# Kernel tuning notes

Hardware: AMD Instinct MI355X
Metric: run time of the kernel (lower is better)

The kernel has to match this reference:

```python
import jax, jax.numpy as jnp
import numpy as np
import math

B, S, H = 2, 2048, 2048
NH, HD = 16, 64  # head_dim = H // (2*NH)
LAMBDA_INIT = 0.5


def setup_inputs() -> dict:
    key = jax.random.key(0)
    ks = jax.random.split(key, 6)
    std = 1.0 / math.sqrt(H)
    hidden_states = jax.random.normal(ks[0], (B, S, H), dtype=jnp.float32)
    # Linear weights stored as [in, out] (x @ W)
    Wq = jax.random.normal(ks[1], (H, 2 * NH * HD), dtype=jnp.float32) * std
    Wk = jax.random.normal(ks[2], (H, 2 * NH * HD), dtype=jnp.float32) * std
    Wv = jax.random.normal(ks[3], (H, NH * HD), dtype=jnp.float32) * std
    Wo = jax.random.normal(ks[4], (NH * HD, H), dtype=jnp.float32) * (1.0 / math.sqrt(NH * HD))
    lambda_param = jnp.log(jnp.asarray(1.0 / math.tanh(LAMBDA_INIT), dtype=jnp.float32))
    # causal additive mask, (B, 1, S, S)
    causal = jnp.tril(jnp.ones((S, S), dtype=bool))
    attention_mask = jnp.where(causal, 0.0, jnp.finfo(jnp.float32).min)[None, None]
    attention_mask = jnp.broadcast_to(attention_mask, (B, 1, S, S))
    return {"hidden_states": hidden_states, "attention_mask": attention_mask,
            "Wq": Wq, "Wk": Wk, "Wv": Wv, "Wo": Wo, "lambda_param": lambda_param}


def reference(hidden_states, attention_mask, Wq, Wk, Wv, Wo, lambda_param):
    bsz, q_len, _ = hidden_states.shape
    scaling = HD ** -0.5

    q_all = (hidden_states @ Wq).reshape(bsz, q_len, 2 * NH, HD).transpose(0, 2, 1, 3)
    k_all = (hidden_states @ Wk).reshape(bsz, q_len, 2 * NH, HD).transpose(0, 2, 1, 3)
    v = (hidden_states @ Wv).reshape(bsz, q_len, NH, HD).transpose(0, 2, 1, 3)
    q1, q2 = q_all[:, :NH], q_all[:, NH:]
    k1, k2 = k_all[:, :NH], k_all[:, NH:]

    lam = jnp.tanh(jax.nn.softplus(lambda_param))
    scores1 = jnp.einsum('bhqd,bhkd->bhqk', q1, k1) * scaling
    scores2 = jnp.einsum('bhqd,bhkd->bhqk', q2, k2) * scaling
    attn_scores = scores1 - lam * scores2 + attention_mask
    attn_weights = jax.nn.softmax(attn_scores.astype(jnp.float32), axis=-1).astype(q1.dtype)

    attn_out = jnp.einsum('bhqk,bhkd->bhqd', attn_weights, v)
    attn_out = attn_out.transpose(0, 2, 1, 3).reshape(bsz, q_len, NH * HD)
    return attn_out @ Wo
```

## Files before the change

kernel.cpp:

```cpp
#include <hip/hip_runtime.h>
#include <hip/hip_bf16.h>

#define B_ 2
#define S_ 2048
#define H_ 2048
#define NH_ 16
#define HD_ 64
#define DQ_ 2048
#define DV_ 1024

using bf16x8 = __attribute__((ext_vector_type(8))) __bf16;
using f32x4  = __attribute__((ext_vector_type(4))) float;

typedef __attribute__((address_space(1))) unsigned int u32g;
typedef __attribute__((address_space(3))) unsigned int u32l;

__device__ __forceinline__ void gload_lds16(const __bf16* g, __bf16* l) {
  __builtin_amdgcn_global_load_lds((u32g*)g, (u32l*)l, 16, 0, 0);
}

__device__ __forceinline__ int swz(int row, int colb, int strideB) {
  return row * strideB + (colb ^ (((row ^ (row >> 3)) & 7) << 4));
}
__device__ __forceinline__ int fxor(int row) { return (row ^ (row >> 3)) & 7; }


__global__ __launch_bounds__(256) void cast_hidden(const float* __restrict__ in,
                                                   __bf16* __restrict__ out, int n) {
  int i = (blockIdx.x * 256 + threadIdx.x) * 8;
  if (i >= n) return;
  float4 a = *reinterpret_cast<const float4*>(in + i);
  float4 b = *reinterpret_cast<const float4*>(in + i + 4);
  bf16x8 o;
  o[0] = (__bf16)a.x; o[1] = (__bf16)a.y; o[2] = (__bf16)a.z; o[3] = (__bf16)a.w;
  o[4] = (__bf16)b.x; o[5] = (__bf16)b.y; o[6] = (__bf16)b.z; o[7] = (__bf16)b.w;
  *reinterpret_cast<bf16x8*>(out + i) = o;
}

__global__ __launch_bounds__(256) void transpose_cast(const float* __restrict__ in,
                                                      __bf16* __restrict__ out, int R, int C) {
  __shared__ float tile[32][33];
  int tx = threadIdx.x & 31, ty = threadIdx.x >> 5;
  int c0 = blockIdx.x * 32, r0 = blockIdx.y * 32;
  for (int i = 0; i < 32; i += 8)
    tile[ty + i][tx] = in[(size_t)(r0 + ty + i) * C + c0 + tx];
  __syncthreads();
  for (int i = 0; i < 32; i += 8)
    out[(size_t)(c0 + ty + i) * R + r0 + tx] = (__bf16)tile[tx][ty + i];
}


template <typename OutT>
__global__ __launch_bounds__(256) void gemm_bt(const __bf16* __restrict__ A,
                                               const __bf16* __restrict__ Bt,
                                               OutT* __restrict__ C,
                                               int M, int N, int K) {
  __shared__ __bf16 As[2][128 * 32];
  __shared__ __bf16 Bs[2][128 * 32];
  const int nx = gridDim.x;
  int id = blockIdx.y * nx + blockIdx.x;
  const int cpx = (nx * gridDim.y) >> 3;
  id = (id & 7) * cpx + (id >> 3);
  const int bm = id / nx, bn = id % nx;

  const int tid = threadIdx.x;
  const int wid = tid >> 6, lane = tid & 63;
  const int wm = wid >> 1, wn = wid & 1;
  const int g = lane >> 4, c = lane & 15;

  f32x4 acc[4][4] = {};
  const __bf16* Abase = A + (size_t)(bm * 128) * K;
  const __bf16* Bbase = Bt + (size_t)(bn * 128) * K;
  const int srow = wid * 16 + (lane >> 2);
  const int scol = (lane & 3) * 8;
  const int nk = K >> 5;

  auto stage = [&](int p, int kt) {
    int k0 = kt * 32;
    gload_lds16(Abase + (size_t)srow * K + k0 + scol,        &As[p][(wid * 16) * 32]);
    gload_lds16(Abase + (size_t)(srow + 64) * K + k0 + scol, &As[p][(64 + wid * 16) * 32]);
    gload_lds16(Bbase + (size_t)srow * K + k0 + scol,        &Bs[p][(wid * 16) * 32]);
    gload_lds16(Bbase + (size_t)(srow + 64) * K + k0 + scol, &Bs[p][(64 + wid * 16) * 32]);
  };

  stage(0, 0);
  stage(1, 1);

  for (int kt = 0; kt < nk; ++kt) {
    const int p = kt & 1;
    if (kt + 1 < nk) {
      asm volatile("s_waitcnt vmcnt(4)" ::: "memory");
    } else {
      asm volatile("s_waitcnt vmcnt(0)" ::: "memory");
    }
    __builtin_amdgcn_s_barrier();
    __builtin_amdgcn_sched_barrier(0);

    bf16x8 af[4], bfv[4];
#pragma unroll
    for (int i = 0; i < 4; ++i)
      af[i] = *reinterpret_cast<const bf16x8*>(&As[p][(wm * 64 + i * 16 + c) * 32 + g * 8]);
#pragma unroll
    for (int i = 0; i < 4; ++i)
      bfv[i] = *reinterpret_cast<const bf16x8*>(&Bs[p][(wn * 64 + i * 16 + c) * 32 + g * 8]);
#pragma unroll
    for (int m = 0; m < 4; ++m)
#pragma unroll
      for (int n = 0; n < 4; ++n)
        acc[m][n] = __builtin_amdgcn_mfma_f32_16x16x32_bf16(af[m], bfv[n], acc[m][n], 0, 0, 0);

    __builtin_amdgcn_sched_barrier(0);
    __builtin_amdgcn_s_barrier();
    if (kt + 2 < nk) stage(p, kt + 2);
  }

#pragma unroll
  for (int m = 0; m < 4; ++m)
#pragma unroll
    for (int n = 0; n < 4; ++n)
#pragma unroll
      for (int r = 0; r < 4; ++r) {
        int row = bm * 128 + wm * 64 + m * 16 + g * 4 + r;
        int col = bn * 128 + wn * 64 + n * 16 + c;
        float v = acc[m][n][r];
        if constexpr (sizeof(OutT) == 2)
          C[(size_t)row * N + col] = (OutT)(__bf16)v;
        else
          C[(size_t)row * N + col] = v;
      }
}


__global__ __launch_bounds__(256, 2) void diffattn(const __bf16* __restrict__ Q,
                                                   const __bf16* __restrict__ Kk,
                                                   const __bf16* __restrict__ V,
                                                   __bf16* __restrict__ O,
                                                   const float* __restrict__ lambda_param) {
  __shared__ __bf16 Ks[2][64 * 128];
  __shared__ __bf16 Vs[2][64 * 64];
  __shared__ __bf16 Ps[128 * 64];

  const int bh = blockIdx.y;
  const int qt = (bh < 16) ? blockIdx.x : (gridDim.x - 1 - blockIdx.x);
  const int b = bh >> 4, h = bh & 15;
  const int tid = threadIdx.x;
  const int w = tid >> 6, lane = tid & 63;
  const int g = lane >> 4, c = lane & 15;

  const float lam = tanhf(log1pf(__expf(lambda_param[0])));
  const float L2E = 1.4426950408889634f;
  const float sc1 = 0.125f * L2E;
  const float sc2 = -lam * 0.125f * L2E;

  bf16x8 qf[2][4];
#pragma unroll
  for (int fr = 0; fr < 2; ++fr) {
    int qrow = qt * 128 + w * 32 + fr * 16 + c;
    const __bf16* qbase = Q + (size_t)(b * S_ + qrow) * DQ_;
#pragma unroll
    for (int kk = 0; kk < 4; ++kk) {
      int d = kk * 32 + g * 8;
      const __bf16* src = (d < 64) ? (qbase + h * 64 + d)
                                   : (qbase + DV_ + h * 64 + (d - 64));
      float s = (d < 64) ? sc1 : sc2;
      bf16x8 raw = *reinterpret_cast<const bf16x8*>(src);
      bf16x8 ov;
#pragma unroll
      for (int i = 0; i < 8; ++i) ov[i] = (__bf16)((float)raw[i] * s);
      qf[fr][kk] = ov;
    }
  }

  f32x4 acc[2][4] = {};
  float mrow[2][4], lrow[2][4];
#pragma unroll
  for (int fr = 0; fr < 2; ++fr)
#pragma unroll
    for (int r = 0; r < 4; ++r) { mrow[fr][r] = -1e30f; lrow[fr][r] = 0.f; }

  const int nt = 2 * qt + 2;

  auto stageK = [&](int p, int kt) {
#pragma unroll
    for (int j = 0; j < 4; ++j) {
      int row = w * 16 + j * 4 + (lane >> 4);
      int gc = (lane & 15) ^ fxor(row);
      int s = kt * 64 + row;
      const __bf16* src = (gc < 8)
          ? (Kk + (size_t)(b * S_ + s) * DQ_ + h * 64 + gc * 8)
          : (Kk + (size_t)(b * S_ + s) * DQ_ + DV_ + h * 64 + (gc - 8) * 8);
      gload_lds16(src, &Ks[p][(w * 16 + j * 4) * 128]);
    }
  };
  auto loadV = [&](int kt, bf16x8* vv) {
#pragma unroll
    for (int j = 0; j < 2; ++j) {
      int flat = tid + j * 256;
      int kv = flat >> 3;
      int d = (flat & 7) * 8;
      vv[j] = *reinterpret_cast<const bf16x8*>(
          V + (size_t)(b * S_ + kt * 64 + kv) * DV_ + h * 64 + d);
    }
  };
  auto scatterV = [&](int p, const bf16x8* vv) {
    char* VsB = (char*)Vs[p];
#pragma unroll
    for (int j = 0; j < 2; ++j) {
      int flat = tid + j * 256;
      int kv = flat >> 3;
      int d = (flat & 7) * 8;
#pragma unroll
      for (int i = 0; i < 8; ++i)
        *reinterpret_cast<__bf16*>(VsB + swz(d + i, kv * 2, 128)) = vv[j][i];
    }
  };

  {
    stageK(0, 0);
    bf16x8 vv[2];
    loadV(0, vv);
    scatterV(0, vv);
    __syncthreads();
  }

  for (int kt = 0; kt < nt; ++kt) {
    const int p = kt & 1;
    const bool pre = (kt + 1 < nt);
    bf16x8 vv[2];
    if (pre) {
      stageK(p ^ 1, kt + 1);
      loadV(kt + 1, vv);
    }

    f32x4 sc[2][4] = {};
    char* KsB = (char*)Ks[p];
    __builtin_amdgcn_s_setprio(1);
#pragma unroll
    for (int f = 0; f < 4; ++f)
#pragma unroll
      for (int kk = 0; kk < 4; ++kk) {
        bf16x8 kf = *reinterpret_cast<const bf16x8*>(
            KsB + swz(f * 16 + c, (kk * 32 + g * 8) * 2, 256));
        sc[0][f] = __builtin_amdgcn_mfma_f32_16x16x32_bf16(qf[0][kk], kf, sc[0][f], 0, 0, 0);
        sc[1][f] = __builtin_amdgcn_mfma_f32_16x16x32_bf16(qf[1][kk], kf, sc[1][f], 0, 0, 0);
      }
    __builtin_amdgcn_s_setprio(0);

    const int dz = kt - 2 * qt;
#pragma unroll
    for (int fr = 0; fr < 2; ++fr) {
      const int wrow0 = w * 32 + fr * 16;
      float pmax[4] = {-1e30f, -1e30f, -1e30f, -1e30f};
      if (dz >= 0) {
#pragma unroll
        for (int f = 0; f < 4; ++f)
#pragma unroll
          for (int r = 0; r < 4; ++r) {
            float s = sc[fr][f][r];
            if (dz * 64 + f * 16 + c > wrow0 + g * 4 + r) s = -1e30f;
            sc[fr][f][r] = s;
            pmax[r] = fmaxf(pmax[r], s);
          }
      } else {
#pragma unroll
        for (int f = 0; f < 4; ++f)
#pragma unroll
          for (int r = 0; r < 4; ++r)
            pmax[r] = fmaxf(pmax[r], sc[fr][f][r]);
      }
#pragma unroll
      for (int m = 1; m < 16; m <<= 1)
#pragma unroll
        for (int r = 0; r < 4; ++r)
          pmax[r] = fmaxf(pmax[r], __shfl_xor(pmax[r], m, 64));

      float dm = -1e30f;
#pragma unroll
      for (int r = 0; r < 4; ++r) dm = fmaxf(dm, pmax[r] - mrow[fr][r]);
      if (!__all(dm <= 8.0f)) {
        float pscl[4];
#pragma unroll
        for (int r = 0; r < 4; ++r) {
          float mnew = fmaxf(mrow[fr][r], pmax[r]);
          pscl[r] = __builtin_amdgcn_exp2f(mrow[fr][r] - mnew);
          mrow[fr][r] = mnew;
        }
#pragma unroll
        for (int r = 0; r < 4; ++r) lrow[fr][r] *= pscl[r];
#pragma unroll
        for (int n = 0; n < 4; ++n)
#pragma unroll
          for (int r = 0; r < 4; ++r)
            acc[fr][n][r] *= pscl[r];
      }

      float rowsum[4] = {0.f, 0.f, 0.f, 0.f};
#pragma unroll
      for (int f = 0; f < 4; ++f)
#pragma unroll
        for (int r = 0; r < 4; ++r) {
          float pv = __builtin_amdgcn_exp2f(sc[fr][f][r] - mrow[fr][r]);
          sc[fr][f][r] = pv;
          rowsum[r] += pv;
        }
#pragma unroll
      for (int m = 1; m < 16; m <<= 1)
#pragma unroll
        for (int r = 0; r < 4; ++r)
          rowsum[r] += __shfl_xor(rowsum[r], m, 64);
#pragma unroll
      for (int r = 0; r < 4; ++r)
        lrow[fr][r] += rowsum[r];

      char* PsB = (char*)Ps;
#pragma unroll
      for (int f = 0; f < 4; ++f)
#pragma unroll
        for (int r = 0; r < 4; ++r)
          *reinterpret_cast<__bf16*>(
              PsB + swz(wrow0 + g * 4 + r, (f * 16 + c) * 2, 128)) = (__bf16)sc[fr][f][r];
    }

    {
      char* PsB = (char*)Ps;
      char* VsB = (char*)Vs[p];
      __builtin_amdgcn_s_setprio(1);
#pragma unroll
      for (int fr = 0; fr < 2; ++fr)
#pragma unroll
        for (int kc = 0; kc < 2; ++kc) {
          bf16x8 pf = *reinterpret_cast<const bf16x8*>(
              PsB + swz(w * 32 + fr * 16 + c, (kc * 32 + g * 8) * 2, 128));
#pragma unroll
          for (int n = 0; n < 4; ++n) {
            bf16x8 vf = *reinterpret_cast<const bf16x8*>(
                VsB + swz(n * 16 + c, (kc * 32 + g * 8) * 2, 128));
            acc[fr][n] = __builtin_amdgcn_mfma_f32_16x16x32_bf16(pf, vf, acc[fr][n], 0, 0, 0);
          }
        }
      __builtin_amdgcn_s_setprio(0);
    }

    if (pre) scatterV(p ^ 1, vv);
    __syncthreads();
  }

#pragma unroll
  for (int fr = 0; fr < 2; ++fr) {
#pragma unroll
    for (int r = 0; r < 4; ++r) lrow[fr][r] = 1.0f / lrow[fr][r];
#pragma unroll
    for (int n = 0; n < 4; ++n)
#pragma unroll
      for (int r = 0; r < 4; ++r) {
        int q = qt * 128 + w * 32 + fr * 16 + g * 4 + r;
        O[(size_t)(b * S_ + q) * DV_ + h * 64 + n * 16 + c] =
            (__bf16)(acc[fr][n][r] * lrow[fr][r]);
      }
  }
}


extern "C" void kernel_launch(void* const* d_in, const int* in_sizes, int n_in,
                              void* d_out, int out_size, void* d_ws, size_t ws_size,
                              hipStream_t stream) {
  const float* hidden = (const float*)d_in[0];
  const float* Wq = (const float*)d_in[2];
  const float* Wk = (const float*)d_in[3];
  const float* Wv = (const float*)d_in[4];
  const float* Wo = (const float*)d_in[5];
  const float* lambda_param = (const float*)d_in[6];
  float* out = (float*)d_out;

  char* ws = (char*)d_ws;
  size_t off = 0;
  auto alloc = [&](size_t bytes) {
    void* p = ws + off;
    off += (bytes + 255) & ~(size_t)255;
    return p;
  };
  const int M = B_ * S_;
  __bf16* hidb = (__bf16*)alloc((size_t)M * H_ * 2);
  __bf16* TB   = (__bf16*)alloc((size_t)H_ * DQ_ * 2);
  __bf16* Qa   = (__bf16*)alloc((size_t)M * DQ_ * 2);
  __bf16* Ka   = (__bf16*)alloc((size_t)M * DQ_ * 2);
  __bf16* Va   = (__bf16*)alloc((size_t)M * DV_ * 2);
  __bf16* AO   = hidb;
  (void)ws_size; (void)in_sizes; (void)n_in; (void)out_size;

  int nh = M * H_;
  cast_hidden<<<nh / (256 * 8), 256, 0, stream>>>(hidden, hidb, nh);

  transpose_cast<<<dim3(DQ_ / 32, H_ / 32), 256, 0, stream>>>(Wq, TB, H_, DQ_);
  gemm_bt<__bf16><<<dim3(DQ_ / 128, M / 128), 256, 0, stream>>>(hidb, TB, Qa, M, DQ_, H_);
  transpose_cast<<<dim3(DQ_ / 32, H_ / 32), 256, 0, stream>>>(Wk, TB, H_, DQ_);
  gemm_bt<__bf16><<<dim3(DQ_ / 128, M / 128), 256, 0, stream>>>(hidb, TB, Ka, M, DQ_, H_);
  transpose_cast<<<dim3(DV_ / 32, H_ / 32), 256, 0, stream>>>(Wv, TB, H_, DV_);
  gemm_bt<__bf16><<<dim3(DV_ / 128, M / 128), 256, 0, stream>>>(hidb, TB, Va, M, DV_, H_);

  diffattn<<<dim3(S_ / 128, B_ * NH_), 256, 0, stream>>>(Qa, Ka, Va, AO, lambda_param);

  transpose_cast<<<dim3(H_ / 32, DV_ / 32), 256, 0, stream>>>(Wo, TB, DV_, H_);
  gemm_bt<float><<<dim3(H_ / 128, M / 128), 256, 0, stream>>>(AO, TB, out, M, H_, DV_);
}
```

Measured before the change: 289.1 us.

## Fuse Q/K projections and switch GEMMs to 256x256 triple-buffered tiles

Replaces the 128x128 double-buffered GEMM with a 512-thread 256x256 tile kernel. It uses three LDS stages, an XOR-swizzled LDS layout, split MFMA phases and s_setprio. The Q and K weights are transposed into one buffer so both projections run as a single GEMM writing an interleaved QK activation, and the attention kernel now reads that layout. The intent is more data reuse per tile and fewer launches. The larger tiles leave the V and output GEMMs with only 64 and 128 blocks on a 256-CU device, which risks poor utilisation.

Measured after the change: 362.0 us. 25.2% more time.

```diff
diff --git a/kernel.cpp b/kernel.cpp
--- a/kernel.cpp
+++ b/kernel.cpp
@@ -8,6 +8,7 @@
 #define HD_ 64
 #define DQ_ 2048
 #define DV_ 1024
+#define QKS_ 4096
 
 using bf16x8 = __attribute__((ext_vector_type(8))) __bf16;
 using f32x4  = __attribute__((ext_vector_type(4))) float;
@@ -23,6 +24,7 @@
   return row * strideB + (colb ^ (((row ^ (row >> 3)) & 7) << 4));
 }
 __device__ __forceinline__ int fxor(int row) { return (row ^ (row >> 3)) & 7; }
+__device__ __forceinline__ int fxor4(int row) { return (row ^ (row >> 2)) & 3; }
 
 
 __global__ __launch_bounds__(256) void cast_hidden(const float* __restrict__ in,
@@ -51,12 +53,13 @@
 
 
 template <typename OutT>
-__global__ __launch_bounds__(256) void gemm_bt(const __bf16* __restrict__ A,
-                                               const __bf16* __restrict__ Bt,
-                                               OutT* __restrict__ C,
-                                               int M, int N, int K) {
-  __shared__ __bf16 As[2][128 * 32];
-  __shared__ __bf16 Bs[2][128 * 32];
+__global__ __launch_bounds__(512, 1) void gemm256(const __bf16* __restrict__ A,
+                                                  const __bf16* __restrict__ Bt,
+                                                  OutT* __restrict__ C,
+                                                  int M, int N, int K) {
+  __shared__ __bf16 As[3][256 * 32];
+  __shared__ __bf16 Bs[3][256 * 32];
+
   const int nx = gridDim.x;
   int id = blockIdx.y * nx + blockIdx.x;
   const int cpx = (nx * gridDim.y) >> 3;
@@ -65,63 +68,98 @@
 
   const int tid = threadIdx.x;
   const int wid = tid >> 6, lane = tid & 63;
-  const int wm = wid >> 1, wn = wid & 1;
+  const int wm = wid >> 2, wn = wid & 3;
   const int g = lane >> 4, c = lane & 15;
 
-  f32x4 acc[4][4] = {};
-  const __bf16* Abase = A + (size_t)(bm * 128) * K;
-  const __bf16* Bbase = Bt + (size_t)(bn * 128) * K;
-  const int srow = wid * 16 + (lane >> 2);
-  const int scol = (lane & 3) * 8;
+  f32x4 acc[8][4] = {};
+  const __bf16* Abase = A + (size_t)(bm * 256) * K;
+  const __bf16* Bbase = Bt + (size_t)(bn * 256) * K;
   const int nk = K >> 5;
 
-  auto stage = [&](int p, int kt) {
-    int k0 = kt * 32;
-    gload_lds16(Abase + (size_t)srow * K + k0 + scol,        &As[p][(wid * 16) * 32]);
-    gload_lds16(Abase + (size_t)(srow + 64) * K + k0 + scol, &As[p][(64 + wid * 16) * 32]);
-    gload_lds16(Bbase + (size_t)srow * K + k0 + scol,        &Bs[p][(wid * 16) * 32]);
-    gload_lds16(Bbase + (size_t)(srow + 64) * K + k0 + scol, &Bs[p][(64 + wid * 16) * 32]);
+  auto stage = [&](int q, int kt) {
+    const int k0 = kt * 32;
+#pragma unroll
+    for (int j = 0; j < 2; ++j) {
+      int flat = tid + j * 512;
+      int row = flat >> 2;
+      int gch = (flat & 3) ^ fxor4(row);
+      __bf16* dst = (__bf16*)&As[q][(wid * 64 + j * 512) * 8];
+      gload_lds16(Abase + (size_t)row * K + k0 + gch * 8, dst);
+    }
+#pragma unroll
+    for (int j = 0; j < 2; ++j) {
+      int flat = tid + j * 512;
+      int row = flat >> 2;
+      int gch = (flat & 3) ^ fxor4(row);
+      __bf16* dst = (__bf16*)&Bs[q][(wid * 64 + j * 512) * 8];
+      gload_lds16(Bbase + (size_t)row * K + k0 + gch * 8, dst);
+    }
+  };
+  auto readA = [&](int q, int m) -> bf16x8 {
+    int row = wm * 128 + m * 16 + c;
+    int ch = g ^ fxor4(row);
+    return *reinterpret_cast<const bf16x8*>(&As[q][row * 32 + ch * 8]);
+  };
+  auto readB = [&](int q, int n) -> bf16x8 {
+    int row = wn * 64 + n * 16 + c;
+    int ch = g ^ fxor4(row);
+    return *reinterpret_cast<const bf16x8*>(&Bs[q][row * 32 + ch * 8]);
   };
 
   stage(0, 0);
   stage(1, 1);
-
-  for (int kt = 0; kt < nk; ++kt) {
-    const int p = kt & 1;
-    if (kt + 1 < nk) {
-      asm volatile("s_waitcnt vmcnt(4)" ::: "memory");
-    } else {
-      asm volatile("s_waitcnt vmcnt(0)" ::: "memory");
-    }
-    __builtin_amdgcn_s_barrier();
-    __builtin_amdgcn_sched_barrier(0);
-
-    bf16x8 af[4], bfv[4];
-#pragma unroll
-    for (int i = 0; i < 4; ++i)
-      af[i] = *reinterpret_cast<const bf16x8*>(&As[p][(wm * 64 + i * 16 + c) * 32 + g * 8]);
-#pragma unroll
-    for (int i = 0; i < 4; ++i)
-      bfv[i] = *reinterpret_cast<const bf16x8*>(&Bs[p][(wn * 64 + i * 16 + c) * 32 + g * 8]);
-#pragma unroll
-    for (int m = 0; m < 4; ++m)
-#pragma unroll
-      for (int n = 0; n < 4; ++n)
-        acc[m][n] = __builtin_amdgcn_mfma_f32_16x16x32_bf16(af[m], bfv[n], acc[m][n], 0, 0, 0);
-
+  asm volatile("s_waitcnt vmcnt(4)" ::: "memory");
+  __builtin_amdgcn_s_barrier();
+
+  for (int t = 0; t < nk; ++t) {
+    const int q = t % 3;
+    if (t + 2 < nk) stage((t + 2) % 3, t + 2);
+
+    bf16x8 bfr[4], afr[4];
+#pragma unroll
+    for (int n = 0; n < 4; ++n) bfr[n] = readB(q, n);
+#pragma unroll
+    for (int m = 0; m < 4; ++m) afr[m] = readA(q, m);
     __builtin_amdgcn_sched_barrier(0);
     __builtin_amdgcn_s_barrier();
-    if (kt + 2 < nk) stage(p, kt + 2);
+    __builtin_amdgcn_s_setprio(1);
+#pragma unroll
+    for (int m = 0; m < 4; ++m)
+#pragma unroll
+      for (int n = 0; n < 4; ++n)
+        acc[m][n] = __builtin_amdgcn_mfma_f32_16x16x32_bf16(afr[m], bfr[n], acc[m][n], 0, 0, 0);
+    __builtin_amdgcn_s_setprio(0);
+    __builtin_amdgcn_sched_barrier(0);
+    __builtin_amdgcn_s_barrier();
+
+#pragma unroll
+    for (int m = 0; m < 4; ++m) afr[m] = readA(q, 4 + m);
+    __builtin_amdgcn_sched_barrier(0);
+    __builtin_amdgcn_s_barrier();
+    __builtin_amdgcn_s_setprio(1);
+#pragma unroll
+    for (int m = 0; m < 4; ++m)
+#pragma unroll
+      for (int n = 0; n < 4; ++n)
+        acc[4 + m][n] = __builtin_amdgcn_mfma_f32_16x16x32_bf16(afr[m], bfr[n], acc[4 + m][n], 0, 0, 0);
+    __builtin_amdgcn_s_setprio(0);
+    __builtin_amdgcn_sched_barrier(0);
+
+    if (t + 1 < nk) {
+      if (t + 2 < nk) asm volatile("s_waitcnt vmcnt(4)" ::: "memory");
+      else            asm volatile("s_waitcnt vmcnt(0)" ::: "memory");
+    }
+    __builtin_amdgcn_s_barrier();
   }
 
 #pragma unroll
-  for (int m = 0; m < 4; ++m)
+  for (int m = 0; m < 8; ++m)
 #pragma unroll
     for (int n = 0; n < 4; ++n)
 #pragma unroll
       for (int r = 0; r < 4; ++r) {
-        int row = bm * 128 + wm * 64 + m * 16 + g * 4 + r;
-        int col = bn * 128 + wn * 64 + n * 16 + c;
+        int row = bm * 256 + wm * 128 + m * 16 + g * 4 + r;
+        int col = bn * 256 + wn * 64 + n * 16 + c;
         float v = acc[m][n][r];
         if constexpr (sizeof(OutT) == 2)
           C[(size_t)row * N + col] = (OutT)(__bf16)v;
@@ -131,8 +169,7 @@
 }
 
 
-__global__ __launch_bounds__(256, 2) void diffattn(const __bf16* __restrict__ Q,
-                                                   const __bf16* __restrict__ Kk,
+__global__ __launch_bounds__(256, 2) void diffattn(const __bf16* __restrict__ QK,
                                                    const __bf16* __restrict__ V,
                                                    __bf16* __restrict__ O,
                                                    const float* __restrict__ lambda_param) {
@@ -156,7 +193,7 @@
 #pragma unroll
   for (int fr = 0; fr < 2; ++fr) {
     int qrow = qt * 128 + w * 32 + fr * 16 + c;
-    const __bf16* qbase = Q + (size_t)(b * S_ + qrow) * DQ_;
+    const __bf16* qbase = QK + (size_t)(b * S_ + qrow) * QKS_;
 #pragma unroll
     for (int kk = 0; kk < 4; ++kk) {
       int d = kk * 32 + g * 8;
@@ -186,9 +223,9 @@
       int row = w * 16 + j * 4 + (lane >> 4);
       int gc = (lane & 15) ^ fxor(row);
       int s = kt * 64 + row;
-      const __bf16* src = (gc < 8)
-          ? (Kk + (size_t)(b * S_ + s) * DQ_ + h * 64 + gc * 8)
-          : (Kk + (size_t)(b * S_ + s) * DQ_ + DV_ + h * 64 + (gc - 8) * 8);
+      const __bf16* kbase = QK + (size_t)(b * S_ + s) * QKS_ + 2048;
+      const __bf16* src = (gc < 8) ? (kbase + h * 64 + gc * 8)
+                                   : (kbase + DV_ + h * 64 + (gc - 8) * 8);
       gload_lds16(src, &Ks[p][(w * 16 + j * 4) * 128]);
     }
   };
@@ -381,10 +418,9 @@
   };
   const int M = B_ * S_;
   __bf16* hidb = (__bf16*)alloc((size_t)M * H_ * 2);
-  __bf16* TB   = (__bf16*)alloc((size_t)H_ * DQ_ * 2);
-  __bf16* Qa   = (__bf16*)alloc((size_t)M * DQ_ * 2);
-  __bf16* Ka   = (__bf16*)alloc((size_t)M * DQ_ * 2);
-  __bf16* Va   = (__bf16*)alloc((size_t)M * DV_ * 2);
+  __bf16* TB   = (__bf16*)alloc((size_t)QKS_ * H_ * 2);
+  __bf16* QKa  = (__bf16*)alloc((size_t)M * QKS_ * 2);
+  __bf16* Va   = (__bf16*)((char*)TB + 4 * 1024 * 1024);
   __bf16* AO   = hidb;
   (void)ws_size; (void)in_sizes; (void)n_in; (void)out_size;
 
@@ -392,14 +428,14 @@
   cast_hidden<<<nh / (256 * 8), 256, 0, stream>>>(hidden, hidb, nh);
 
   transpose_cast<<<dim3(DQ_ / 32, H_ / 32), 256, 0, stream>>>(Wq, TB, H_, DQ_);
-  gemm_bt<__bf16><<<dim3(DQ_ / 128, M / 128), 256, 0, stream>>>(hidb, TB, Qa, M, DQ_, H_);
-  transpose_cast<<<dim3(DQ_ / 32, H_ / 32), 256, 0, stream>>>(Wk, TB, H_, DQ_);
-  gemm_bt<__bf16><<<dim3(DQ_ / 128, M / 128), 256, 0, stream>>>(hidb, TB, Ka, M, DQ_, H_);
+  transpose_cast<<<dim3(DQ_ / 32, H_ / 32), 256, 0, stream>>>(Wk, TB + (size_t)DQ_ * H_, H_, DQ_);
+  gemm256<__bf16><<<dim3(QKS_ / 256, M / 256), 512, 0, stream>>>(hidb, TB, QKa, M, QKS_, H_);
+
   transpose_cast<<<dim3(DV_ / 32, H_ / 32), 256, 0, stream>>>(Wv, TB, H_, DV_);
-  gemm_bt<__bf16><<<dim3(DV_ / 128, M / 128), 256, 0, stream>>>(hidb, TB, Va, M, DV_, H_);
-
-  diffattn<<<dim3(S_ / 128, B_ * NH_), 256, 0, stream>>>(Qa, Ka, Va, AO, lambda_param);
+  gemm256<__bf16><<<dim3(DV_ / 256, M / 256), 512, 0, stream>>>(hidb, TB, Va, M, DV_, H_);
+
+  diffattn<<<dim3(S_ / 128, B_ * NH_), 256, 0, stream>>>(QKa, Va, AO, lambda_param);
 
   transpose_cast<<<dim3(H_ / 32, DV_ / 32), 256, 0, stream>>>(Wo, TB, DV_, H_);
-  gemm_bt<float><<<dim3(H_ / 128, M / 128), 256, 0, stream>>>(AO, TB, out, M, H_, DV_);
-}
+  gemm256<float><<<dim3(H_ / 256, M / 256), 512, 0, stream>>>(AO, TB, out, M, H_, DV_);
+}
```

## Split causal attention over key range into two halves and fuse QK projections

Applied to the files above, without the earlier changes.

The differential attention kernel now splits each query tile's key range into two halves run as separate blocks. Each block writes an unnormalized partial output plus its row max and sum, and a new merge kernel combines the halves with a log-sum-exp rescale. This doubles the block count and evens out the causal workload imbalance, at the cost of extra partial-output memory traffic and one more launch. The Q and K projections are also fused into one wider GEMM over concatenated transposed weights, with workspace buffers re-aliased to fit.

New measurement: 316.6 us. 1.1x slower.

```diff
diff --git a/kernel.cpp b/kernel.cpp
--- a/kernel.cpp
+++ b/kernel.cpp
@@ -8,6 +8,7 @@
 #define HD_ 64
 #define DQ_ 2048
 #define DV_ 1024
+#define QKS_ 4096
 
 using bf16x8 = __attribute__((ext_vector_type(8))) __bf16;
 using f32x4  = __attribute__((ext_vector_type(4))) float;
@@ -131,21 +132,24 @@
 }
 
 
-__global__ __launch_bounds__(256, 2) void diffattn(const __bf16* __restrict__ Q,
-                                                   const __bf16* __restrict__ Kk,
+__global__ __launch_bounds__(256, 2) void diffattn(const __bf16* __restrict__ QK,
                                                    const __bf16* __restrict__ V,
-                                                   __bf16* __restrict__ O,
+                                                   __bf16* __restrict__ OpA,
+                                                   __bf16* __restrict__ OpB,
+                                                   float* __restrict__ ml,
                                                    const float* __restrict__ lambda_param) {
   __shared__ __bf16 Ks[2][64 * 128];
   __shared__ __bf16 Vs[2][64 * 64];
   __shared__ __bf16 Ps[128 * 64];
 
-  const int bh = blockIdx.y;
-  const int qt = (bh < 16) ? blockIdx.x : (gridDim.x - 1 - blockIdx.x);
+  const int qt = (gridDim.x - 1) - blockIdx.x;
+  const int bh = blockIdx.y >> 1;
+  const int half = blockIdx.y & 1;
   const int b = bh >> 4, h = bh & 15;
   const int tid = threadIdx.x;
   const int w = tid >> 6, lane = tid & 63;
   const int g = lane >> 4, c = lane & 15;
+  const float NEG_INF = -__builtin_inff();
 
   const float lam = tanhf(log1pf(__expf(lambda_param[0])));
   const float L2E = 1.4426950408889634f;
@@ -156,7 +160,7 @@
 #pragma unroll
   for (int fr = 0; fr < 2; ++fr) {
     int qrow = qt * 128 + w * 32 + fr * 16 + c;
-    const __bf16* qbase = Q + (size_t)(b * S_ + qrow) * DQ_;
+    const __bf16* qbase = QK + (size_t)(b * S_ + qrow) * QKS_;
 #pragma unroll
     for (int kk = 0; kk < 4; ++kk) {
       int d = kk * 32 + g * 8;
@@ -178,7 +182,8 @@
 #pragma unroll
     for (int r = 0; r < 4; ++r) { mrow[fr][r] = -1e30f; lrow[fr][r] = 0.f; }
 
-  const int nt = 2 * qt + 2;
+  const int kt0 = half ? (qt + 1) : 0;
+  const int kt1 = half ? (2 * qt + 2) : (qt + 1);
 
   auto stageK = [&](int p, int kt) {
 #pragma unroll
@@ -186,9 +191,9 @@
       int row = w * 16 + j * 4 + (lane >> 4);
       int gc = (lane & 15) ^ fxor(row);
       int s = kt * 64 + row;
-      const __bf16* src = (gc < 8)
-          ? (Kk + (size_t)(b * S_ + s) * DQ_ + h * 64 + gc * 8)
-          : (Kk + (size_t)(b * S_ + s) * DQ_ + DV_ + h * 64 + (gc - 8) * 8);
+      const __bf16* kbase = QK + (size_t)(b * S_ + s) * QKS_ + 2048;
+      const __bf16* src = (gc < 8) ? (kbase + h * 64 + gc * 8)
+                                   : (kbase + DV_ + h * 64 + (gc - 8) * 8);
       gload_lds16(src, &Ks[p][(w * 16 + j * 4) * 128]);
     }
   };
@@ -216,16 +221,16 @@
   };
 
   {
-    stageK(0, 0);
+    stageK(0, kt0);
     bf16x8 vv[2];
-    loadV(0, vv);
+    loadV(kt0, vv);
     scatterV(0, vv);
     __syncthreads();
   }
 
-  for (int kt = 0; kt < nt; ++kt) {
-    const int p = kt & 1;
-    const bool pre = (kt + 1 < nt);
+  for (int kt = kt0; kt < kt1; ++kt) {
+    const int p = (kt - kt0) & 1;
+    const bool pre = (kt + 1 < kt1);
     bf16x8 vv[2];
     if (pre) {
       stageK(p ^ 1, kt + 1);
@@ -257,7 +262,7 @@
 #pragma unroll
           for (int r = 0; r < 4; ++r) {
             float s = sc[fr][f][r];
-            if (dz * 64 + f * 16 + c > wrow0 + g * 4 + r) s = -1e30f;
+            if (dz * 64 + f * 16 + c > wrow0 + g * 4 + r) s = NEG_INF;
             sc[fr][f][r] = s;
             pmax[r] = fmaxf(pmax[r], s);
           }
@@ -274,7 +279,7 @@
         for (int r = 0; r < 4; ++r)
           pmax[r] = fmaxf(pmax[r], __shfl_xor(pmax[r], m, 64));
 
-      float dm = -1e30f;
+      float dm = NEG_INF;
 #pragma unroll
       for (int r = 0; r < 4; ++r) dm = fmaxf(dm, pmax[r] - mrow[fr][r]);
       if (!__all(dm <= 8.0f)) {
@@ -345,19 +350,57 @@
     __syncthreads();
   }
 
-#pragma unroll
-  for (int fr = 0; fr < 2; ++fr) {
-#pragma unroll
-    for (int r = 0; r < 4; ++r) lrow[fr][r] = 1.0f / lrow[fr][r];
+  __bf16* Op = half ? OpB : OpA;
+#pragma unroll
+  for (int fr = 0; fr < 2; ++fr)
 #pragma unroll
     for (int n = 0; n < 4; ++n)
 #pragma unroll
       for (int r = 0; r < 4; ++r) {
         int q = qt * 128 + w * 32 + fr * 16 + g * 4 + r;
-        O[(size_t)(b * S_ + q) * DV_ + h * 64 + n * 16 + c] =
-            (__bf16)(acc[fr][n][r] * lrow[fr][r]);
+        Op[(size_t)(b * S_ + q) * DV_ + h * 64 + n * 16 + c] = (__bf16)acc[fr][n][r];
+      }
+  if (c == 0) {
+#pragma unroll
+    for (int fr = 0; fr < 2; ++fr)
+#pragma unroll
+      for (int r = 0; r < 4; ++r) {
+        int q = qt * 128 + w * 32 + fr * 16 + g * 4 + r;
+        float2 v;
+        v.x = mrow[fr][r];
+        v.y = lrow[fr][r];
+        *reinterpret_cast<float2*>(&ml[((size_t)(half * 32 + bh) * S_ + q) * 2]) = v;
       }
   }
+}
+
+
+__global__ __launch_bounds__(256) void merge_halves(const __bf16* __restrict__ OpA,
+                                                    const __bf16* __restrict__ OpB,
+                                                    const float* __restrict__ ml,
+                                                    __bf16* __restrict__ AO) {
+  int flat = blockIdx.x * 256 + threadIdx.x;
+  int d0 = (flat & 7) * 8;
+  int row = flat >> 3;
+  int bh = row >> 11, q = row & 2047;
+  int b = bh >> 4, h = bh & 15;
+  size_t obase = (size_t)(b * S_ + q) * DV_ + h * 64 + d0;
+
+  float2 a2 = *reinterpret_cast<const float2*>(&ml[((size_t)bh * S_ + q) * 2]);
+  float2 b2 = *reinterpret_cast<const float2*>(&ml[((size_t)(32 + bh) * S_ + q) * 2]);
+  float m = fmaxf(a2.x, b2.x);
+  float wA = __builtin_amdgcn_exp2f(a2.x - m);
+  float wB = __builtin_amdgcn_exp2f(b2.x - m);
+  float inv = 1.0f / (a2.y * wA + b2.y * wB);
+  wA *= inv; wB *= inv;
+
+  bf16x8 oa = *reinterpret_cast<const bf16x8*>(OpA + obase);
+  bf16x8 ob = *reinterpret_cast<const bf16x8*>(OpB + obase);
+  bf16x8 o;
+#pragma unroll
+  for (int i = 0; i < 8; ++i)
+    o[i] = (__bf16)((float)oa[i] * wA + (float)ob[i] * wB);
+  *reinterpret_cast<bf16x8*>(AO + obase) = o;
 }
 
 
@@ -381,10 +424,12 @@
   };
   const int M = B_ * S_;
   __bf16* hidb = (__bf16*)alloc((size_t)M * H_ * 2);
-  __bf16* TB   = (__bf16*)alloc((size_t)H_ * DQ_ * 2);
-  __bf16* Qa   = (__bf16*)alloc((size_t)M * DQ_ * 2);
-  __bf16* Ka   = (__bf16*)alloc((size_t)M * DQ_ * 2);
-  __bf16* Va   = (__bf16*)alloc((size_t)M * DV_ * 2);
+  __bf16* TB   = (__bf16*)alloc((size_t)QKS_ * H_ * 2);
+  __bf16* QKa  = (__bf16*)alloc((size_t)M * QKS_ * 2);
+  __bf16* Va   = (__bf16*)((char*)TB + 4u * 1024 * 1024);
+  float*  mlb  = (float*)((char*)TB + 12u * 1024 * 1024);
+  __bf16* OpA  = hidb;
+  __bf16* OpB  = hidb + (size_t)M * DV_;
   __bf16* AO   = hidb;
   (void)ws_size; (void)in_sizes; (void)n_in; (void)out_size;
 
@@ -392,13 +437,14 @@
   cast_hidden<<<nh / (256 * 8), 256, 0, stream>>>(hidden, hidb, nh);
 
   transpose_cast<<<dim3(DQ_ / 32, H_ / 32), 256, 0, stream>>>(Wq, TB, H_, DQ_);
-  gemm_bt<__bf16><<<dim3(DQ_ / 128, M / 128), 256, 0, stream>>>(hidb, TB, Qa, M, DQ_, H_);
-  transpose_cast<<<dim3(DQ_ / 32, H_ / 32), 256, 0, stream>>>(Wk, TB, H_, DQ_);
-  gemm_bt<__bf16><<<dim3(DQ_ / 128, M / 128), 256, 0, stream>>>(hidb, TB, Ka, M, DQ_, H_);
+  transpose_cast<<<dim3(DQ_ / 32, H_ / 32), 256, 0, stream>>>(Wk, TB + (size_t)DQ_ * H_, H_, DQ_);
+  gemm_bt<__bf16><<<dim3(QKS_ / 128, M / 128), 256, 0, stream>>>(hidb, TB, QKa, M, QKS_, H_);
+
   transpose_cast<<<dim3(DV_ / 32, H_ / 32), 256, 0, stream>>>(Wv, TB, H_, DV_);
   gemm_bt<__bf16><<<dim3(DV_ / 128, M / 128), 256, 0, stream>>>(hidb, TB, Va, M, DV_, H_);
 
-  diffattn<<<dim3(S_ / 128, B_ * NH_), 256, 0, stream>>>(Qa, Ka, Va, AO, lambda_param);
+  diffattn<<<dim3(S_ / 128, B_ * NH_ * 2), 256, 0, stream>>>(QKa, Va, OpA, OpB, mlb, lambda_param);
+  merge_halves<<<(B_ * NH_ * S_ * HD_ / 8) / 256, 256, 0, stream>>>(OpA, OpB, mlb, AO);
 
   transpose_cast<<<dim3(H_ / 32, DV_ / 32), 256, 0, stream>>>(Wo, TB, DV_, H_);
   gemm_bt<float><<<dim3(H_ / 128, M / 128), 256, 0, stream>>>(AO, TB, out, M, H_, DV_);
```
